# Kernel tuning notes

Measured on AMD Instinct MI355X. Metric: run time of the kernel, lower is better.

## Reference

```python
import jax, jax.numpy as jnp
import numpy as np

B, D_IN, D_OUT = 32768, 256, 256
E, H, GH, K = 8, 512, 128, 2
BALANCE_COEF = 0.01


def setup_inputs() -> dict:
    key = jax.random.key(0)
    ks = jax.random.split(key, 12)
    def w(k, shape, fan_in):
        return jax.random.normal(k, shape, jnp.float32) / np.sqrt(fan_in)
    return {
        "x":   jax.random.normal(ks[0], (B, D_IN), jnp.float32),
        # gating network params
        "gW1": w(ks[1], (D_IN, GH), D_IN), "gb1": jnp.zeros((GH,), jnp.float32),
        "gW2": w(ks[2], (GH, E), GH),      "gb2": jnp.zeros((E,), jnp.float32),
        # expert MLP params, stacked over experts: Linear->ReLU->Linear->ReLU->Linear
        "We1": w(ks[3], (E, D_IN, H), D_IN), "be1": jnp.zeros((E, H), jnp.float32),
        "We2": w(ks[4], (E, H, H), H),       "be2": jnp.zeros((E, H), jnp.float32),
        "We3": w(ks[5], (E, H, D_OUT), H),   "be3": jnp.zeros((E, D_OUT), jnp.float32),
    }


def reference(x, gW1, gb1, gW2, gb2, We1, be1, We2, be2, We3, be3):
    # Gating: MLP -> softmax -> top-k -> renormalize (eval mode: no noise, no dropout)
    logits = jnp.maximum(x @ gW1 + gb1, 0.0) @ gW2 + gb2          # [B, E]
    probs = jax.nn.softmax(logits, axis=-1)
    w, idx = jax.lax.top_k(probs, K)                              # [B, K] each
    w = w / jnp.sum(w, axis=-1, keepdims=True)
    onehot = jax.nn.one_hot(idx, E, dtype=x.dtype)                # [B, K, E]
    cw = jnp.einsum('bk,bke->be', w, onehot)                      # combine weights [B, E]

    # Expert compute + weighted combine. Loop over small fixed expert count;
    # cw is zero for unselected (token, expert) pairs, matching the masked
    # gather/scatter math of the original exactly.
    out = jnp.zeros((x.shape[0], We3.shape[-1]), x.dtype)
    for e in range(E):
        h = jnp.maximum(x @ We1[e] + be1[e], 0.0)                 # [B, H]
        h = jnp.maximum(h @ We2[e] + be2[e], 0.0)                 # [B, H]
        y = h @ We3[e] + be3[e]                                   # [B, D_OUT]
        out = out + y * cw[:, e:e + 1]

    # Aux: expert usage = sum over k slots of mean_b(indices==e)
    expert_usage = jnp.mean(jnp.sum(onehot, axis=1), axis=0)      # [E]
    balance_loss = jnp.mean((expert_usage - 1.0 / E) ** 2) * BALANCE_COEF
    return out, balance_loss, expert_usage
```

## Files before the change

### kernel.cpp

```cpp
#include <hip/hip_runtime.h>
#include <stdint.h>

#define E_ 8
#define DIN 256
#define DOUT 256
#define HID 512
#define GHID 128
#define NTOK 32768
#define NROW (NTOK * 2)
#define TABCAP 520
#define CNT_STRIDE 32

typedef float f32x4 __attribute__((ext_vector_type(4)));
typedef short bf16x8 __attribute__((ext_vector_type(8)));

__device__ __forceinline__ unsigned short f2bf(float f) {
    unsigned int u = __float_as_uint(f);
    u += 0x7FFFu + ((u >> 16) & 1u);
    return (unsigned short)(u >> 16);
}

__device__ __forceinline__ void gload_lds16(const void* g, void* l) {
    __builtin_amdgcn_global_load_lds(
        (const __attribute__((address_space(1))) unsigned int*)g,
        (__attribute__((address_space(3))) unsigned int*)l, 16, 0, 0);
}

__global__ __launch_bounds__(256) void k_transpose_bf16(
    const float* __restrict__ src, unsigned short* __restrict__ dst, int K, int N) {
    __shared__ float tile[64][65];
    int e = blockIdx.z;
    int k0 = blockIdx.x * 64, n0 = blockIdx.y * 64;
    const float* s = src + (size_t)e * K * N;
    unsigned short* d = dst + (size_t)e * N * K;
    int col = threadIdx.x & 63, ri = threadIdx.x >> 6;
#pragma unroll
    for (int it = 0; it < 16; ++it) {
        int row = it * 4 + ri;
        tile[row][col] = s[(size_t)(k0 + row) * N + n0 + col];
    }
    __syncthreads();
#pragma unroll
    for (int it = 0; it < 16; ++it) {
        int nrow = it * 4 + ri;
        d[(size_t)(n0 + nrow) * K + k0 + col] = f2bf(tile[col][nrow]);
    }
}

__global__ __launch_bounds__(256) void k_gate1(
    const float* __restrict__ x, const float* __restrict__ gW1,
    const float* __restrict__ gb1, float* __restrict__ hG) {
    __shared__ float xT[32][132];
    __shared__ float ws[32][132];
    int t = threadIdx.x;
    int tokBase = blockIdx.x * 128;
    int tx = t & 15, ty = t >> 4;
    float acc[8][8];
#pragma unroll
    for (int i = 0; i < 8; ++i)
#pragma unroll
        for (int j = 0; j < 8; ++j) acc[i][j] = 0.f;

    int stok = t >> 1;
    int skh = (t & 1) * 16;
    int wkk = t >> 3;
    int wh = (t & 7) * 16;

    for (int k0 = 0; k0 < DIN; k0 += 32) {
        const float* xr = x + (size_t)(tokBase + stok) * DIN + k0 + skh;
        float4 a0 = ((const float4*)xr)[0];
        float4 a1 = ((const float4*)xr)[1];
        float4 a2 = ((const float4*)xr)[2];
        float4 a3 = ((const float4*)xr)[3];
        xT[skh + 0][stok] = a0.x;  xT[skh + 1][stok] = a0.y;
        xT[skh + 2][stok] = a0.z;  xT[skh + 3][stok] = a0.w;
        xT[skh + 4][stok] = a1.x;  xT[skh + 5][stok] = a1.y;
        xT[skh + 6][stok] = a1.z;  xT[skh + 7][stok] = a1.w;
        xT[skh + 8][stok] = a2.x;  xT[skh + 9][stok] = a2.y;
        xT[skh + 10][stok] = a2.z; xT[skh + 11][stok] = a2.w;
        xT[skh + 12][stok] = a3.x; xT[skh + 13][stok] = a3.y;
        xT[skh + 14][stok] = a3.z; xT[skh + 15][stok] = a3.w;
        const float* wr = gW1 + (size_t)(k0 + wkk) * GHID + wh;
        *(float4*)&ws[wkk][wh + 0]  = ((const float4*)wr)[0];
        *(float4*)&ws[wkk][wh + 4]  = ((const float4*)wr)[1];
        *(float4*)&ws[wkk][wh + 8]  = ((const float4*)wr)[2];
        *(float4*)&ws[wkk][wh + 12] = ((const float4*)wr)[3];
        __syncthreads();
#pragma unroll 4
        for (int kk = 0; kk < 32; ++kk) {
            f32x4 wv0 = *(const f32x4*)&ws[kk][tx * 8];
            f32x4 wv1 = *(const f32x4*)&ws[kk][tx * 8 + 4];
            f32x4 xv0 = *(const f32x4*)&xT[kk][ty * 8];
            f32x4 xv1 = *(const f32x4*)&xT[kk][ty * 8 + 4];
            float xs[8] = {xv0.x, xv0.y, xv0.z, xv0.w, xv1.x, xv1.y, xv1.z, xv1.w};
            float wsv[8] = {wv0.x, wv0.y, wv0.z, wv0.w, wv1.x, wv1.y, wv1.z, wv1.w};
#pragma unroll
            for (int i = 0; i < 8; ++i)
#pragma unroll
                for (int j = 0; j < 8; ++j) acc[i][j] += xs[i] * wsv[j];
        }
        __syncthreads();
    }
    float4 b0 = *(const float4*)&gb1[tx * 8];
    float4 b1 = *(const float4*)&gb1[tx * 8 + 4];
#pragma unroll
    for (int i = 0; i < 8; ++i) {
        int tok = tokBase + ty * 8 + i;
        float4 o0, o1;
        o0.x = fmaxf(acc[i][0] + b0.x, 0.f); o0.y = fmaxf(acc[i][1] + b0.y, 0.f);
        o0.z = fmaxf(acc[i][2] + b0.z, 0.f); o0.w = fmaxf(acc[i][3] + b0.w, 0.f);
        o1.x = fmaxf(acc[i][4] + b1.x, 0.f); o1.y = fmaxf(acc[i][5] + b1.y, 0.f);
        o1.z = fmaxf(acc[i][6] + b1.z, 0.f); o1.w = fmaxf(acc[i][7] + b1.w, 0.f);
        float* hr = &hG[(size_t)tok * GHID + tx * 8];
        ((float4*)hr)[0] = o0;
        ((float4*)hr)[1] = o1;
    }
}

__global__ __launch_bounds__(256) void k_gate2(
    const float* __restrict__ hG, const float* __restrict__ gW2,
    const float* __restrict__ gb2, int2* __restrict__ tokE,
    float2* __restrict__ tokW, int* __restrict__ cnt) {
    __shared__ float hs[64][132];
    __shared__ float wg[GHID * E_];
    __shared__ int lcnt[E_];
    int t = threadIdx.x;
    int tokBase = blockIdx.x * 64;
#pragma unroll
    for (int i = 0; i < 4; ++i) wg[i * 256 + t] = gW2[i * 256 + t];
    if (t < E_) lcnt[t] = 0;
#pragma unroll
    for (int it = 0; it < 8; ++it) {
        int idx = it * 256 + t;
        int tok = idx >> 5, col = (idx & 31) * 4;
        float4 v = *(const float4*)&hG[(size_t)(tokBase + tok) * GHID + col];
        *(float4*)&hs[tok][col] = v;
    }
    __syncthreads();
    int tok = t >> 2, part = t & 3;
    float s[8];
#pragma unroll
    for (int e = 0; e < E_; ++e) s[e] = 0.f;
    const float* hr = &hs[tok][part * 32];
#pragma unroll 2
    for (int jq = 0; jq < 8; ++jq) {
        f32x4 hv = *(const f32x4*)&hr[jq * 4];
#pragma unroll
        for (int j = 0; j < 4; ++j) {
            float h = hv[j];
            int hidx = part * 32 + jq * 4 + j;
            f32x4 w0 = *(const f32x4*)&wg[hidx * 8];
            f32x4 w1 = *(const f32x4*)&wg[hidx * 8 + 4];
            s[0] += h * w0.x; s[1] += h * w0.y; s[2] += h * w0.z; s[3] += h * w0.w;
            s[4] += h * w1.x; s[5] += h * w1.y; s[6] += h * w1.z; s[7] += h * w1.w;
        }
    }
#pragma unroll
    for (int e = 0; e < E_; ++e) {
        s[e] += __shfl_xor(s[e], 1);
        s[e] += __shfl_xor(s[e], 2);
    }
    if (part == 0) {
        float l[8];
#pragma unroll
        for (int e = 0; e < E_; ++e) l[e] = s[e] + gb2[e];
        int i1 = 0; float b1v = l[0];
#pragma unroll
        for (int e = 1; e < E_; ++e) if (l[e] > b1v) { b1v = l[e]; i1 = e; }
        int i2 = -1; float b2v = -3.4e38f;
#pragma unroll
        for (int e = 0; e < E_; ++e) if (e != i1 && l[e] > b2v) { b2v = l[e]; i2 = e; }
        float mm = fmaxf(b1v, b2v);
        float p1 = expf(b1v - mm), p2 = expf(b2v - mm);
        float inv = 1.f / (p1 + p2);
        int gtok = tokBase + tok;
        tokE[gtok] = make_int2(i1, i2);
        tokW[gtok] = make_float2(p1 * inv, p2 * inv);
        atomicAdd(&lcnt[i1], 1);
        atomicAdd(&lcnt[i2], 1);
    }
    __syncthreads();
    if (t < E_) atomicAdd(&cnt[t * CNT_STRIDE], lcnt[t]);
}

__global__ void k_route_setup(const int* __restrict__ cnt, int* __restrict__ offs,
                              int* __restrict__ fill, int2* __restrict__ tab,
                              int* __restrict__ NT, float* __restrict__ outTail) {
    int t = threadIdx.x;
    int c[E_], nt[E_];
#pragma unroll
    for (int e = 0; e < E_; ++e) {
        c[e] = cnt[e * CNT_STRIDE];
        nt[e] = (c[e] + 127) >> 7;
    }
    if (t == 0) {
        int off = 0, ntp = 0;
        float bl = 0.f;
#pragma unroll
        for (int e = 0; e < E_; ++e) {
            offs[e] = off; off += c[e];
            fill[e] = 0;
            ntp += nt[e];
            float u = (float)c[e] / 32768.f;
            outTail[8388609 + e] = u;
            float dd = u - 0.125f;
            bl += dd * dd;
        }
        outTail[8388608] = bl * (0.01f / 8.f);
        *NT = ntp;
    }
    int maxnt = 0;
#pragma unroll
    for (int e = 0; e < E_; ++e) maxnt = max(maxnt, nt[e]);
    for (int k = t; k < maxnt; k += 64) {
        int p = 0;
#pragma unroll
        for (int e = 0; e < E_; ++e) p += min(nt[e], k);
#pragma unroll
        for (int e = 0; e < E_; ++e) {
            if (k < nt[e]) {
                tab[p] = make_int2(e, k);
                ++p;
            }
        }
    }
}

__global__ __launch_bounds__(256) void k_gather(
    const float* __restrict__ x, const int2* __restrict__ tokE,
    const float2* __restrict__ tokW, const int* __restrict__ offs,
    int* __restrict__ fill, int* __restrict__ rowTok, float* __restrict__ rowW,
    unsigned short* __restrict__ xg) {
    __shared__ int lc[E_], lbase[E_], lfill[E_];
    __shared__ int srow[512];
    int t = threadIdx.x;
    int tokBase = blockIdx.x * 256;
    if (t < E_) { lc[t] = 0; lfill[t] = 0; }
    __syncthreads();
    for (int s = t; s < 512; s += 256) {
        int token = tokBase + (s >> 1);
        int2 ee = tokE[token];
        int e = (s & 1) ? ee.y : ee.x;
        atomicAdd(&lc[e], 1);
    }
    __syncthreads();
    if (t < E_) lbase[t] = atomicAdd(&fill[t], lc[t]);
    __syncthreads();
    for (int s = t; s < 512; s += 256) {
        int token = tokBase + (s >> 1);
        int2 ee = tokE[token];
        float2 wv = tokW[token];
        int e; float w;
        if (s & 1) { e = ee.y; w = wv.y; } else { e = ee.x; w = wv.x; }
        int r = atomicAdd(&lfill[e], 1);
        int row = offs[e] + lbase[e] + r;
        srow[s] = row;
        rowTok[row] = token;
        rowW[row] = w;
    }
    __syncthreads();
    int wid = t >> 6, lane = t & 63;
    for (int s = wid; s < 512; s += 4) {
        int row = srow[s];
        int token = tokBase + (s >> 1);
        float4 v = ((const float4*)x)[(size_t)token * 64 + lane];
        ushort4 o;
        o.x = f2bf(v.x); o.y = f2bf(v.y); o.z = f2bf(v.z); o.w = f2bf(v.w);
        ((ushort4*)xg)[(size_t)row * 64 + lane] = o;
    }
}

template <int NCT>
__global__ __launch_bounds__(512, 4) void k_gemm(
    const unsigned short* __restrict__ A, const unsigned short* __restrict__ BT,
    const float* __restrict__ bias, const int* __restrict__ offs,
    const int* __restrict__ cnt, const int2* __restrict__ tab,
    const int* __restrict__ NT, int N, int K, int mode,
    unsigned short* __restrict__ Hout, float* __restrict__ outF,
    const int* __restrict__ rowTok, const float* __restrict__ rowW) {
    __shared__ __align__(16) unsigned short As[3][128 * 32];
    __shared__ __align__(16) unsigned short Bs[3][128 * 32];

    unsigned flat = blockIdx.x + (unsigned)NCT * blockIdx.y;
    unsigned xcd = flat % 8u;
    unsigned q = flat / 8u;
    unsigned ct = q % (unsigned)NCT;
    unsigned tIdx = (q / (unsigned)NCT) * 8u + xcd;

    if (tIdx >= (unsigned)*NT || tIdx >= (unsigned)TABCAP) return;
    int2 ent = tab[tIdx];
    int e = ent.x, rt = ent.y;
    int cntE = cnt[e * CNT_STRIDE];
    int rowStart = offs[e] + rt * 128;
    int valid = cntE - rt * 128;
    if (valid > 128) valid = 128;

    int t = threadIdx.x;
    int lane = t & 63, wid = t >> 6;
    int quad = lane >> 4, l15 = lane & 15;
    int waveM = wid >> 2, waveN = wid & 3;

    const unsigned short* Ablk = A + (size_t)rowStart * K;
    const unsigned short* Bblk = BT + ((size_t)e * N + (size_t)ct * 128) * K;

    int srow = t >> 2, skc = t & 3;
    int skcs = skc ^ ((srow >> 1) & 3);
    int ar = min(srow, valid - 1);
    const unsigned short* ga = Ablk + (size_t)ar * K + skcs * 8;
    const unsigned short* gb = Bblk + (size_t)srow * K + skcs * 8;
    int la = wid * 512;

    auto stage = [&](int b, int kt) {
        gload_lds16(ga + kt, &As[b][la]);
        gload_lds16(gb + kt, &Bs[b][la]);
    };

    const f32x4 zero = {0.f, 0.f, 0.f, 0.f};
    f32x4 acc[4][2];
#pragma unroll
    for (int i = 0; i < 4; ++i)
#pragma unroll
        for (int j = 0; j < 2; ++j) acc[i][j] = zero;

    int xq = quad ^ ((l15 >> 1) & 3);
    int nst = K >> 5;
    stage(0, 0);
    stage(1, 32);
    int bs = 0;
    for (int s = 0; s < nst; ++s) {
        if (s + 1 < nst) {
            asm volatile("s_waitcnt vmcnt(2)" ::: "memory");
        } else {
            asm volatile("s_waitcnt vmcnt(0)" ::: "memory");
        }
        __builtin_amdgcn_s_barrier();
        asm volatile("" ::: "memory");
        if (s + 2 < nst) {
            int b2 = bs + 2; if (b2 >= 3) b2 -= 3;
            stage(b2, (s + 2) << 5);
        }
        const unsigned short* Ab = As[bs];
        const unsigned short* Bb = Bs[bs];
        bf16x8 af[4], bf[2];
#pragma unroll
        for (int i = 0; i < 4; ++i)
            af[i] = *(const bf16x8*)&Ab[(waveM * 64 + i * 16 + l15) * 32 + xq * 8];
#pragma unroll
        for (int j = 0; j < 2; ++j)
            bf[j] = *(const bf16x8*)&Bb[(waveN * 32 + j * 16 + l15) * 32 + xq * 8];
#pragma unroll
        for (int i = 0; i < 4; ++i)
#pragma unroll
            for (int j = 0; j < 2; ++j)
                acc[i][j] = __builtin_amdgcn_mfma_f32_16x16x32_bf16(af[i], bf[j], acc[i][j], 0, 0, 0);
        ++bs; if (bs == 3) bs = 0;
    }

    const float* be = bias + (size_t)e * N;
    if (mode == 0) {
#pragma unroll
        for (int i = 0; i < 4; ++i) {
#pragma unroll
            for (int r = 0; r < 4; ++r) {
                int rl = waveM * 64 + i * 16 + quad * 4 + r;
                if (rl < valid) {
                    size_t rowOff = (size_t)(rowStart + rl) * N;
#pragma unroll
                    for (int j = 0; j < 2; ++j) {
                        int col = (int)ct * 128 + waveN * 32 + j * 16 + l15;
                        float v = acc[i][j][r] + be[col];
                        Hout[rowOff + col] = f2bf(fmaxf(v, 0.f));
                    }
                }
            }
        }
    } else {
#pragma unroll
        for (int i = 0; i < 4; ++i) {
#pragma unroll
            for (int r = 0; r < 4; ++r) {
                int rl = waveM * 64 + i * 16 + quad * 4 + r;
                if (rl < valid) {
                    int row = rowStart + rl;
                    int tok = rowTok[row];
                    float w = rowW[row];
                    float* orow = outF + (size_t)tok * DOUT;
#pragma unroll
                    for (int j = 0; j < 2; ++j) {
                        int col = (int)ct * 128 + waveN * 32 + j * 16 + l15;
                        float v = (acc[i][j][r] + be[col]) * w;
                        atomicAdd(&orow[col], v);
                    }
                }
            }
        }
    }
}

extern "C" void kernel_launch(void* const* d_in, const int* in_sizes, int n_in,
                              void* d_out, int out_size, void* d_ws, size_t ws_size,
                              hipStream_t stream) {
    const float* x   = (const float*)d_in[0];
    const float* gW1 = (const float*)d_in[1];
    const float* gb1 = (const float*)d_in[2];
    const float* gW2 = (const float*)d_in[3];
    const float* gb2 = (const float*)d_in[4];
    const float* We1 = (const float*)d_in[5];
    const float* be1 = (const float*)d_in[6];
    const float* We2 = (const float*)d_in[7];
    const float* be2 = (const float*)d_in[8];
    const float* We3 = (const float*)d_in[9];
    const float* be3 = (const float*)d_in[10];
    float* out = (float*)d_out;

    uint8_t* ws = (uint8_t*)d_ws;
    size_t off = 0;
    auto alloc = [&](size_t bytes) -> void* {
        void* p = ws + off;
        off += (bytes + 255) & ~(size_t)255;
        return p;
    };
    unsigned short* WT1 = (unsigned short*)alloc((size_t)E_ * HID * DIN * 2);
    unsigned short* WT2 = (unsigned short*)alloc((size_t)E_ * HID * HID * 2);
    unsigned short* WT3 = (unsigned short*)alloc((size_t)E_ * DOUT * HID * 2);
    unsigned short* R1  = (unsigned short*)alloc((size_t)NROW * HID * 2);
    unsigned short* h1  = (unsigned short*)alloc((size_t)NROW * HID * 2);
    float*  hG     = (float*)alloc((size_t)NTOK * GHID * 4);
    int2*   tokE   = (int2*)alloc((size_t)NTOK * 8);
    float2* tokW   = (float2*)alloc((size_t)NTOK * 8);
    int*    rowTok = (int*)alloc((size_t)NROW * 4);
    float*  rowW   = (float*)alloc((size_t)NROW * 4);
    int*    cnt    = (int*)alloc(E_ * CNT_STRIDE * 4);
    int*    offs   = (int*)alloc(256);
    int*    fill   = (int*)alloc(256);
    int*    NT     = (int*)alloc(256);
    int2*   tab    = (int2*)alloc(TABCAP * 8);
    unsigned short* xg = R1;
    unsigned short* h2 = R1;

    hipMemsetAsync(d_out, 0, (size_t)out_size * 4, stream);
    hipMemsetAsync(cnt, 0, E_ * CNT_STRIDE * 4, stream);

    k_transpose_bf16<<<dim3(DIN / 64, HID / 64, E_), 256, 0, stream>>>(We1, WT1, DIN, HID);
    k_transpose_bf16<<<dim3(HID / 64, HID / 64, E_), 256, 0, stream>>>(We2, WT2, HID, HID);
    k_transpose_bf16<<<dim3(HID / 64, DOUT / 64, E_), 256, 0, stream>>>(We3, WT3, HID, DOUT);

    k_gate1<<<NTOK / 128, 256, 0, stream>>>(x, gW1, gb1, hG);
    k_gate2<<<NTOK / 64, 256, 0, stream>>>(hG, gW2, gb2, tokE, tokW, cnt);
    k_route_setup<<<1, 64, 0, stream>>>(cnt, offs, fill, tab, NT, out);
    k_gather<<<NTOK / 256, 256, 0, stream>>>(x, tokE, tokW, offs, fill, rowTok, rowW, xg);

    k_gemm<4><<<dim3(4, TABCAP), 512, 0, stream>>>(xg, WT1, be1, offs, cnt, tab, NT,
                                                   HID, DIN, 0, h1, nullptr, rowTok, rowW);
    k_gemm<4><<<dim3(4, TABCAP), 512, 0, stream>>>(h1, WT2, be2, offs, cnt, tab, NT,
                                                   HID, HID, 0, h2, nullptr, rowTok, rowW);
    k_gemm<2><<<dim3(2, TABCAP), 512, 0, stream>>>(h2, WT3, be3, offs, cnt, tab, NT,
                                                   DOUT, HID, 1, nullptr, out, rowTok, rowW);
}
```

Measured before the change: 389.8 us.

## Replace atomic scatter-add in final GEMM with row store plus combine kernel

The last expert GEMM now writes un-weighted per-row outputs into a dense fp32 buffer (reusing the h1 region) instead of doing weighted atomicAdds into the output. A new combine kernel reads each token's two rows through a token-to-row map recorded during gather and writes the weighted sum directly. This removes the output memset and the float atomics. In exchange it adds an extra kernel launch and a write and reread of a 64K x 256 fp32 intermediate. The combine also fixes the summation order, making results deterministic.

```diff
diff --git a/kernel.cpp b/kernel.cpp
--- a/kernel.cpp
+++ b/kernel.cpp
@@ -230,7 +230,7 @@
     const float* __restrict__ x, const int2* __restrict__ tokE,
     const float2* __restrict__ tokW, const int* __restrict__ offs,
     int* __restrict__ fill, int* __restrict__ rowTok, float* __restrict__ rowW,
-    unsigned short* __restrict__ xg) {
+    int2* __restrict__ tokRow, unsigned short* __restrict__ xg) {
     __shared__ int lc[E_], lbase[E_], lfill[E_];
     __shared__ int srow[512];
     int t = threadIdx.x;
@@ -257,6 +257,7 @@
         srow[s] = row;
         rowTok[row] = token;
         rowW[row] = w;
+        ((int*)&tokRow[token])[s & 1] = row;
     }
     __syncthreads();
     int wid = t >> 6, lane = t & 63;
@@ -381,20 +382,34 @@
             for (int r = 0; r < 4; ++r) {
                 int rl = waveM * 64 + i * 16 + quad * 4 + r;
                 if (rl < valid) {
-                    int row = rowStart + rl;
-                    int tok = rowTok[row];
-                    float w = rowW[row];
-                    float* orow = outF + (size_t)tok * DOUT;
+                    float* yrow = outF + (size_t)(rowStart + rl) * N;
 #pragma unroll
                     for (int j = 0; j < 2; ++j) {
                         int col = (int)ct * 128 + waveN * 32 + j * 16 + l15;
-                        float v = (acc[i][j][r] + be[col]) * w;
-                        atomicAdd(&orow[col], v);
+                        yrow[col] = acc[i][j][r] + be[col];
                     }
                 }
             }
         }
     }
+}
+
+__global__ __launch_bounds__(256) void k_combine(
+    const float* __restrict__ y, const int2* __restrict__ tokRow,
+    const float* __restrict__ rowW, float* __restrict__ out) {
+    int gid = blockIdx.x * 256 + threadIdx.x;
+    int tok = gid >> 6;
+    int cg = (gid & 63) << 2;
+    int2 rr = tokRow[tok];
+    float w0 = rowW[rr.x], w1 = rowW[rr.y];
+    float4 a = *(const float4*)&y[(size_t)rr.x * DOUT + cg];
+    float4 b = *(const float4*)&y[(size_t)rr.y * DOUT + cg];
+    float4 o;
+    o.x = w0 * a.x + w1 * b.x;
+    o.y = w0 * a.y + w1 * b.y;
+    o.z = w0 * a.z + w1 * b.z;
+    o.w = w0 * a.w + w1 * b.w;
+    *(float4*)&out[(size_t)tok * DOUT + cg] = o;
 }
 
 extern "C" void kernel_launch(void* const* d_in, const int* in_sizes, int n_in,
@@ -430,6 +445,7 @@
     float2* tokW   = (float2*)alloc((size_t)NTOK * 8);
     int*    rowTok = (int*)alloc((size_t)NROW * 4);
     float*  rowW   = (float*)alloc((size_t)NROW * 4);
+    int2*   tokRow = (int2*)alloc((size_t)NTOK * 8);
     int*    cnt    = (int*)alloc(E_ * CNT_STRIDE * 4);
     int*    offs   = (int*)alloc(256);
     int*    fill   = (int*)alloc(256);
@@ -437,8 +453,8 @@
     int2*   tab    = (int2*)alloc(TABCAP * 8);
     unsigned short* xg = R1;
     unsigned short* h2 = R1;
-
-    hipMemsetAsync(d_out, 0, (size_t)out_size * 4, stream);
+    float* y = (float*)h1;
+
     hipMemsetAsync(cnt, 0, E_ * CNT_STRIDE * 4, stream);
 
     k_transpose_bf16<<<dim3(DIN / 64, HID / 64, E_), 256, 0, stream>>>(We1, WT1, DIN, HID);
@@ -448,12 +464,14 @@
     k_gate1<<<NTOK / 128, 256, 0, stream>>>(x, gW1, gb1, hG);
     k_gate2<<<NTOK / 64, 256, 0, stream>>>(hG, gW2, gb2, tokE, tokW, cnt);
     k_route_setup<<<1, 64, 0, stream>>>(cnt, offs, fill, tab, NT, out);
-    k_gather<<<NTOK / 256, 256, 0, stream>>>(x, tokE, tokW, offs, fill, rowTok, rowW, xg);
+    k_gather<<<NTOK / 256, 256, 0, stream>>>(x, tokE, tokW, offs, fill, rowTok, rowW,
+                                             tokRow, xg);
 
     k_gemm<4><<<dim3(4, TABCAP), 512, 0, stream>>>(xg, WT1, be1, offs, cnt, tab, NT,
                                                    HID, DIN, 0, h1, nullptr, rowTok, rowW);
     k_gemm<4><<<dim3(4, TABCAP), 512, 0, stream>>>(h1, WT2, be2, offs, cnt, tab, NT,
                                                    HID, HID, 0, h2, nullptr, rowTok, rowW);
     k_gemm<2><<<dim3(2, TABCAP), 512, 0, stream>>>(h2, WT3, be3, offs, cnt, tab, NT,
-                                                   DOUT, HID, 1, nullptr, out, rowTok, rowW);
-}
+                                                   DOUT, HID, 1, nullptr, y, rowTok, rowW);
+    k_combine<<<NTOK * DOUT / 4 / 256, 256, 0, stream>>>(y, tokRow, rowW, out);
+}
```

After: 355.7 us. -8.7%, faster.
